# Kernel optimization log

Measured on AMD Instinct MI355X. Metric: run time of the kernel, lower is better.

## Reference

```python
import jax, jax.numpy as jnp
import numpy as np

NDIM = 3        # coordinate dimensionality
KS = 3          # kernel size per dim (odd)
DIL = 0.05      # dilation (spacing between kernel cells)
MAXD = 1.0      # max_distance cap on SDF values
G = 64          # SDF grid resolution per dim
NSDF = 8        # number of SDF grids
OUT = 32        # out_channels
K = KS ** NDIM  # 27 kernel cells
CELL = 0.031    # grid cell size -> grid extent ~2.0


def _kernel_offsets():
    r = (jnp.arange(KS, dtype=jnp.float32) - KS // 2) * DIL
    ox, oy, oz = jnp.meshgrid(r, r, r, indexing='ij')
    return jnp.stack([ox.ravel(), oy.ravel(), oz.ravel()], -1)  # [K,3]


def _rot_inv(q, v):
    # rotate v by the inverse of quaternion q (xyzw layout), broadcasting
    u = -q[..., :3]
    w = q[..., 3:4]
    c = jnp.cross(u, v)
    return v + 2.0 * jnp.cross(u, c + w * v)


def setup_inputs() -> dict:
    key = jax.random.key(0)
    ks = jax.random.split(key, 8)
    B, N, M = 2, 50000, 4
    extent = G * CELL  # ~2.0, local grid extent
    locs = jax.random.uniform(ks[0], (B, N, NDIM), jnp.float32) * extent
    idxs = jax.random.randint(ks[1], (B, M), 0, NSDF).astype(jnp.int32)
    trans = jax.random.uniform(ks[2], (B, M, NDIM), jnp.float32) * 0.2
    quat = jax.random.normal(ks[3], (B, M, 4), jnp.float32)
    quat = quat / jnp.linalg.norm(quat, axis=-1, keepdims=True)
    poses = jnp.concatenate([trans, quat], axis=-1)  # [B,M,7] = trans + quat(xyzw)
    scales = jax.random.uniform(ks[4], (B, M), jnp.float32) + 0.5
    sdf_grid = jax.random.normal(ks[5], (NSDF, G, G, G), jnp.float32) * 0.3 + 0.2
    cell_sizes = jnp.full((NSDF,), CELL, jnp.float32)
    weight = jax.random.normal(ks[6], (OUT, K), jnp.float32) * 0.1
    bias = jax.random.normal(ks[7], (OUT,), jnp.float32) * 0.1
    return dict(locs=locs, idxs=idxs, poses=poses, scales=scales,
                sdf_grid=sdf_grid, cell_sizes=cell_sizes, weight=weight, bias=bias)


def _convsdf(locs, idxs, poses, scales, sdf_grid, cell_sizes, weight, bias):
    offs = _kernel_offsets()                                  # [K,3]
    p = locs[:, :, None, :] + offs[None, None, :, :]          # [B,N,K,3] kernel-cell points
    t = poses[:, :, :NDIM]                                    # [B,M,3]
    q = poses[:, :, NDIM:]                                    # [B,M,4]
    # transform each kernel-cell point into each SDF's local frame
    r = p[:, :, :, None, :] - t[:, None, None, :, :]          # [B,N,K,M,3]
    r = _rot_inv(q[:, None, None, :, :], r)
    sc = scales[:, None, None, :, None]                       # [B,1,1,M,1]
    r = r / sc
    cs = cell_sizes[idxs][:, None, None, :, None]             # [B,1,1,M,1]
    gc = r / cs - 0.5                                         # grid coords (values at cell centers)
    inb = jnp.all((r >= 0.0) & (r <= G * cs), axis=-1)        # [B,N,K,M] inside grid?
    gcc = jnp.clip(gc, 0.0, G - 1.0)
    i0 = jnp.clip(jnp.floor(gcc), 0.0, G - 2.0).astype(jnp.int32)
    fr = gcc - i0.astype(jnp.float32)
    flat = sdf_grid.reshape(-1)
    jb = idxs.astype(jnp.int32)[:, None, None, :]             # [B,1,1,M]
    val = jnp.zeros(inb.shape, jnp.float32)
    # trilinear interpolation: 8 corner gathers
    for dx in (0, 1):
        wx = fr[..., 0] if dx else 1.0 - fr[..., 0]
        for dy in (0, 1):
            wy = fr[..., 1] if dy else 1.0 - fr[..., 1]
            for dz in (0, 1):
                wz = fr[..., 2] if dz else 1.0 - fr[..., 2]
                fi = ((jb * G + i0[..., 0] + dx) * G + i0[..., 1] + dy) * G + i0[..., 2] + dz
                val = val + wx * wy * wz * jnp.take(flat, fi)
    # scaled SDF value; out-of-grid -> max_distance, then min over objects, cap
    val = jnp.where(inb, val * sc[..., 0], MAXD)
    d = jnp.minimum(jnp.min(val, axis=-1), MAXD)              # [B,N,K]
    return jnp.einsum('bnk,ok->bno', d, weight) + bias        # [B,N,OUT]


def reference(locs, idxs, poses, scales, sdf_grid, cell_sizes, weight, bias):
    return _convsdf(locs, idxs, poses, scales, sdf_grid, cell_sizes, weight, bias)
```

## Files before the change

kernel.cpp:

```cpp
#include <hip/hip_runtime.h>
#include <hip/hip_fp16.h>
#include <math.h>

#define KK 27
#define MM 4
#define OUTC 32
#define GG 64
#define GG3 (GG * GG * GG)
#define DILF 0.05f
#define MAXDF 1.0f
#define MU 4e-3f

static __device__ inline bool exact_inb(float lx, float ly, float lz,
                                        float ox, float oy, float oz,
                                        float tx, float ty, float tz,
                                        float qx, float qy, float qz, float qw,
                                        float sc, float gcs) {
#pragma clang fp contract(off)
    float px = lx + ox, py = ly + oy, pz = lz + oz;
    float vx = px - tx, vy = py - ty, vz = pz - tz;
    float ux = -qx, uy = -qy, uz = -qz;
    float cx = uy * vz - uz * vy;
    float cy = uz * vx - ux * vz;
    float cz = ux * vy - uy * vx;
    float twx = cx + qw * vx;
    float twy = cy + qw * vy;
    float twz = cz + qw * vz;
    float rx = vx + 2.0f * (uy * twz - uz * twy);
    float ry = vy + 2.0f * (uz * twx - ux * twz);
    float rz = vz + 2.0f * (ux * twy - uy * twx);
    rx = rx / sc; ry = ry / sc; rz = rz / sc;
    return (rx >= 0.0f) & (rx <= gcs) & (ry >= 0.0f) & (ry <= gcs) &
           (rz >= 0.0f) & (rz <= gcs);
}

__global__ __launch_bounds__(256) void repack_kernel(
    const float* __restrict__ sdf, const int* __restrict__ idxs,
    uint2* __restrict__ quad, int nslots) {
    const int j = blockIdx.y;
    __shared__ int ref;
    if (threadIdx.x == 0) {
        int r = 0;
        for (int s = 0; s < nslots; ++s) r |= (idxs[s] == j) ? 1 : 0;
        ref = r;
    }
    __syncthreads();
    if (!ref) return;

    int i = blockIdx.x * 256 + threadIdx.x;
    int x = i >> 12, y = (i >> 6) & 63, z = i & 63;
    int xp = min(x + 1, 63), zp = min(z + 1, 63);
    const float* g = sdf + (size_t)j * GG3;
    float v000 = g[(x * GG + y) * GG + z];
    float v001 = g[(x * GG + y) * GG + zp];
    float v100 = g[(xp * GG + y) * GG + z];
    float v101 = g[(xp * GG + y) * GG + zp];
    __half2 h0 = __floats2half2_rn(v000, v001);
    __half2 h1 = __floats2half2_rn(v100, v101);
    uint2 o;
    o.x = *(unsigned int*)&h0;
    o.y = *(unsigned int*)&h1;
    quad[(size_t)j * GG3 + i] = o;
}

__global__ __launch_bounds__(256) void convsdf_quad_kernel(
    const float* __restrict__ locs, const int* __restrict__ idxs,
    const float* __restrict__ poses, const float* __restrict__ scales,
    const uint2* __restrict__ quad, const float* __restrict__ cells,
    const float* __restrict__ weight, const float* __restrict__ bias,
    float* __restrict__ out, int N) {
    __shared__ float4 s_ro[MM][KK];
    __shared__ float4 s_off[KK];
    __shared__ float4 s_wT4[KK * OUTC / 4];
    __shared__ float  s_bias[OUTC];
    __shared__ float  s_t[MM][3];
    __shared__ float  s_q[MM][4];
    __shared__ float  s_sc[MM];
    __shared__ float  s_gcs[MM];
    __shared__ float  s_invscs[MM];
    __shared__ int    s_goff[MM];

    const int b = blockIdx.y;
    const int tid = threadIdx.x;

    float* s_wT = (float*)s_wT4;
    for (int i = tid; i < KK * OUTC; i += 256) {
        int k = i >> 5, o = i & 31;
        s_wT[i] = weight[o * KK + k];
    }
    if (tid < OUTC) s_bias[tid] = bias[tid];
    if (tid < KK) {
        int kx = tid / 9, ky = (tid / 3) % 3, kz = tid % 3;
        s_off[tid] = make_float4((float)(kx - 1) * DILF, (float)(ky - 1) * DILF,
                                 (float)(kz - 1) * DILF, 0.0f);
    }
    if (tid >= 128 && tid < 128 + MM) {
        int m = tid - 128;
        const float* pp = poses + (b * MM + m) * 7;
        float sc = scales[b * MM + m];
        int gi = idxs[b * MM + m];
        float cs = cells[gi];
        s_t[m][0] = pp[0]; s_t[m][1] = pp[1]; s_t[m][2] = pp[2];
        s_q[m][0] = pp[3]; s_q[m][1] = pp[4]; s_q[m][2] = pp[5]; s_q[m][3] = pp[6];
        s_sc[m] = sc;
        s_gcs[m] = (float)GG * cs;
        s_invscs[m] = 1.0f / (sc * cs);
        s_goff[m] = gi * GG3;
    }
    __syncthreads();

    if (tid < MM * KK) {
        int m = tid / KK, k = tid - m * KK;
        float4 off = s_off[k];
        float qx = s_q[m][0], qy = s_q[m][1], qz = s_q[m][2], qw = s_q[m][3];
        float ux = -qx, uy = -qy, uz = -qz;
        float vx = off.x, vy = off.y, vz = off.z;
        float cx = uy * vz - uz * vy + qw * vx;
        float cy = uz * vx - ux * vz + qw * vy;
        float cz = ux * vy - uy * vx + qw * vz;
        float rx = vx + 2.0f * (uy * cz - uz * cy);
        float ry = vy + 2.0f * (uz * cx - ux * cz);
        float rz = vz + 2.0f * (ux * cy - uy * cx);
        float f = s_invscs[m];
        s_ro[m][k] = make_float4(rx * f, ry * f, rz * f, 0.0f);
    }
    __syncthreads();

    const int pl = tid >> 2;
    const int m  = tid & 3;
    const int n  = blockIdx.x * 64 + pl;
    if (n >= N) return;

    const float* lp = locs + (size_t)(b * N + n) * 3;
    float lx = lp[0], ly = lp[1], lz = lp[2];

    float tx = s_t[m][0], ty = s_t[m][1], tz = s_t[m][2];
    float qx = s_q[m][0], qy = s_q[m][1], qz = s_q[m][2], qw = s_q[m][3];
    float sc = s_sc[m], gcs = s_gcs[m];
    float bux, buy, buz;
    {
        float vx = lx - tx, vy = ly - ty, vz = lz - tz;
        float ux = -qx, uy = -qy, uz = -qz;
        float cx = uy * vz - uz * vy + qw * vx;
        float cy = uz * vx - ux * vz + qw * vy;
        float cz = ux * vy - uy * vx + qw * vz;
        float rx = vx + 2.0f * (uy * cz - uz * cy);
        float ry = vy + 2.0f * (uz * cx - ux * cz);
        float rz = vz + 2.0f * (ux * cy - uy * cx);
        float f = s_invscs[m];
        bux = rx * f; buy = ry * f; buz = rz * f;
    }
    const uint2* qg = quad + s_goff[m];

    float acc[8];
#pragma unroll
    for (int j = 0; j < 8; ++j) acc[j] = s_bias[m * 8 + j];

#pragma unroll 3
    for (int k = 0; k < KK; ++k) {
        float4 ro = s_ro[m][k];
        float ux = bux + ro.x;
        float uy = buy + ro.y;
        float uz = buz + ro.z;
        float mn = fminf(fminf(ux, uy), uz);
        float mx = fmaxf(fmaxf(ux, uy), uz);
        bool inb = (mn >= 0.0f) & (mx <= 64.0f);
        float a0 = fminf(fminf(fabsf(ux), fabsf(uy)), fabsf(uz));
        float a1 = fminf(fminf(fabsf(ux - 64.0f), fabsf(uy - 64.0f)),
                         fabsf(uz - 64.0f));
        if (fminf(a0, a1) < MU) {
            float4 ofk = s_off[k];
            inb = exact_inb(lx, ly, lz, ofk.x, ofk.y, ofk.z,
                            tx, ty, tz, qx, qy, qz, qw, sc, gcs);
        }
        float v = MAXDF;
        if (inb) {
            float gx = fminf(fmaxf(ux - 0.5f, 0.0f), 63.0f);
            float gy = fminf(fmaxf(uy - 0.5f, 0.0f), 63.0f);
            float gz = fminf(fmaxf(uz - 0.5f, 0.0f), 63.0f);
            int ix = min((int)gx, 62);
            int iy = min((int)gy, 62);
            int iz = min((int)gz, 62);
            float fx = gx - (float)ix;
            float fy = gy - (float)iy;
            float fz = gz - (float)iz;
            int base = (ix * GG + iy) * GG + iz;
            uint2 qa = qg[base];
            uint2 qb = qg[base + GG];
            float2 az  = __half22float2(*(__half2*)&qa.x);
            float2 axz = __half22float2(*(__half2*)&qa.y);
            float2 bz  = __half22float2(*(__half2*)&qb.x);
            float2 bxz = __half22float2(*(__half2*)&qb.y);
            float c00 = az.x  + fz * (az.y  - az.x);
            float c10 = axz.x + fz * (axz.y - axz.x);
            float c01 = bz.x  + fz * (bz.y  - bz.x);
            float c11 = bxz.x + fz * (bxz.y - bxz.x);
            float c0 = c00 + fy * (c01 - c00);
            float c1 = c10 + fy * (c11 - c10);
            v = (c0 + fx * (c1 - c0)) * sc;
        }
        float dk = v;
        dk = fminf(dk, __shfl_xor(dk, 1, 4));
        dk = fminf(dk, __shfl_xor(dk, 2, 4));
        float4 w0 = s_wT4[k * (OUTC / 4) + m * 2 + 0];
        float4 w1 = s_wT4[k * (OUTC / 4) + m * 2 + 1];
        acc[0] += dk * w0.x; acc[1] += dk * w0.y;
        acc[2] += dk * w0.z; acc[3] += dk * w0.w;
        acc[4] += dk * w1.x; acc[5] += dk * w1.y;
        acc[6] += dk * w1.z; acc[7] += dk * w1.w;
    }

    float* op = out + (size_t)(b * N + n) * OUTC + m * 8;
    *(float4*)&op[0] = make_float4(acc[0], acc[1], acc[2], acc[3]);
    *(float4*)&op[4] = make_float4(acc[4], acc[5], acc[6], acc[7]);
}

__global__ __launch_bounds__(256) void convsdf_direct_kernel(
    const float* __restrict__ locs, const int* __restrict__ idxs,
    const float* __restrict__ poses, const float* __restrict__ scales,
    const float* __restrict__ sdf, const float* __restrict__ cells,
    const float* __restrict__ weight, const float* __restrict__ bias,
    float* __restrict__ out, int N) {
    __shared__ float4 s_ro[MM][KK];
    __shared__ float4 s_off[KK];
    __shared__ float4 s_wT4[KK * OUTC / 4];
    __shared__ float  s_bias[OUTC];
    __shared__ float  s_t[MM][3];
    __shared__ float  s_q[MM][4];
    __shared__ float  s_sc[MM];
    __shared__ float  s_gcs[MM];
    __shared__ float  s_invscs[MM];
    __shared__ int    s_goff[MM];

    const int b = blockIdx.y;
    const int tid = threadIdx.x;

    float* s_wT = (float*)s_wT4;
    for (int i = tid; i < KK * OUTC; i += 256) {
        int k = i >> 5, o = i & 31;
        s_wT[i] = weight[o * KK + k];
    }
    if (tid < OUTC) s_bias[tid] = bias[tid];
    if (tid < KK) {
        int kx = tid / 9, ky = (tid / 3) % 3, kz = tid % 3;
        s_off[tid] = make_float4((float)(kx - 1) * DILF, (float)(ky - 1) * DILF,
                                 (float)(kz - 1) * DILF, 0.0f);
    }
    if (tid >= 128 && tid < 128 + MM) {
        int m = tid - 128;
        const float* pp = poses + (b * MM + m) * 7;
        float sc = scales[b * MM + m];
        int gi = idxs[b * MM + m];
        float cs = cells[gi];
        s_t[m][0] = pp[0]; s_t[m][1] = pp[1]; s_t[m][2] = pp[2];
        s_q[m][0] = pp[3]; s_q[m][1] = pp[4]; s_q[m][2] = pp[5]; s_q[m][3] = pp[6];
        s_sc[m] = sc;
        s_gcs[m] = (float)GG * cs;
        s_invscs[m] = 1.0f / (sc * cs);
        s_goff[m] = gi * GG3;
    }
    __syncthreads();

    if (tid < MM * KK) {
        int m = tid / KK, k = tid - m * KK;
        float4 off = s_off[k];
        float qx = s_q[m][0], qy = s_q[m][1], qz = s_q[m][2], qw = s_q[m][3];
        float ux = -qx, uy = -qy, uz = -qz;
        float vx = off.x, vy = off.y, vz = off.z;
        float cx = uy * vz - uz * vy + qw * vx;
        float cy = uz * vx - ux * vz + qw * vy;
        float cz = ux * vy - uy * vx + qw * vz;
        float rx = vx + 2.0f * (uy * cz - uz * cy);
        float ry = vy + 2.0f * (uz * cx - ux * cz);
        float rz = vz + 2.0f * (ux * cy - uy * cx);
        float f = s_invscs[m];
        s_ro[m][k] = make_float4(rx * f, ry * f, rz * f, 0.0f);
    }
    __syncthreads();

    const int pl = tid >> 2;
    const int m  = tid & 3;
    const int n  = blockIdx.x * 64 + pl;
    if (n >= N) return;

    const float* lp = locs + (size_t)(b * N + n) * 3;
    float lx = lp[0], ly = lp[1], lz = lp[2];

    float tx = s_t[m][0], ty = s_t[m][1], tz = s_t[m][2];
    float qx = s_q[m][0], qy = s_q[m][1], qz = s_q[m][2], qw = s_q[m][3];
    float sc = s_sc[m], gcs = s_gcs[m];
    float bux, buy, buz;
    {
        float vx = lx - tx, vy = ly - ty, vz = lz - tz;
        float ux = -qx, uy = -qy, uz = -qz;
        float cx = uy * vz - uz * vy + qw * vx;
        float cy = uz * vx - ux * vz + qw * vy;
        float cz = ux * vy - uy * vx + qw * vz;
        float rx = vx + 2.0f * (uy * cz - uz * cy);
        float ry = vy + 2.0f * (uz * cx - ux * cz);
        float rz = vz + 2.0f * (ux * cy - uy * cx);
        float f = s_invscs[m];
        bux = rx * f; buy = ry * f; buz = rz * f;
    }
    const float* gbase = sdf + s_goff[m];

    float acc[8];
#pragma unroll
    for (int j = 0; j < 8; ++j) acc[j] = s_bias[m * 8 + j];

#pragma unroll 3
    for (int k = 0; k < KK; ++k) {
        float4 ro = s_ro[m][k];
        float ux = bux + ro.x;
        float uy = buy + ro.y;
        float uz = buz + ro.z;
        float mn = fminf(fminf(ux, uy), uz);
        float mx = fmaxf(fmaxf(ux, uy), uz);
        bool inb = (mn >= 0.0f) & (mx <= 64.0f);
        float a0 = fminf(fminf(fabsf(ux), fabsf(uy)), fabsf(uz));
        float a1 = fminf(fminf(fabsf(ux - 64.0f), fabsf(uy - 64.0f)),
                         fabsf(uz - 64.0f));
        if (fminf(a0, a1) < MU) {
            float4 ofk = s_off[k];
            inb = exact_inb(lx, ly, lz, ofk.x, ofk.y, ofk.z,
                            tx, ty, tz, qx, qy, qz, qw, sc, gcs);
        }
        float v = MAXDF;
        if (inb) {
            float gx = fminf(fmaxf(ux - 0.5f, 0.0f), 63.0f);
            float gy = fminf(fmaxf(uy - 0.5f, 0.0f), 63.0f);
            float gz = fminf(fmaxf(uz - 0.5f, 0.0f), 63.0f);
            int ix = min((int)gx, 62);
            int iy = min((int)gy, 62);
            int iz = min((int)gz, 62);
            float fx = gx - (float)ix;
            float fy = gy - (float)iy;
            float fz = gz - (float)iz;
            const float* g = gbase + ((ix * GG + iy) * GG + iz);
            float v000 = g[0], v001 = g[1];
            float v010 = g[GG], v011 = g[GG + 1];
            float v100 = g[GG * GG], v101 = g[GG * GG + 1];
            float v110 = g[GG * GG + GG], v111 = g[GG * GG + GG + 1];
            float c00 = v000 + fz * (v001 - v000);
            float c01 = v010 + fz * (v011 - v010);
            float c10 = v100 + fz * (v101 - v100);
            float c11 = v110 + fz * (v111 - v110);
            float c0 = c00 + fy * (c01 - c00);
            float c1 = c10 + fy * (c11 - c10);
            v = (c0 + fx * (c1 - c0)) * sc;
        }
        float dk = v;
        dk = fminf(dk, __shfl_xor(dk, 1, 4));
        dk = fminf(dk, __shfl_xor(dk, 2, 4));
        float4 w0 = s_wT4[k * (OUTC / 4) + m * 2 + 0];
        float4 w1 = s_wT4[k * (OUTC / 4) + m * 2 + 1];
        acc[0] += dk * w0.x; acc[1] += dk * w0.y;
        acc[2] += dk * w0.z; acc[3] += dk * w0.w;
        acc[4] += dk * w1.x; acc[5] += dk * w1.y;
        acc[6] += dk * w1.z; acc[7] += dk * w1.w;
    }

    float* op = out + (size_t)(b * N + n) * OUTC + m * 8;
    *(float4*)&op[0] = make_float4(acc[0], acc[1], acc[2], acc[3]);
    *(float4*)&op[4] = make_float4(acc[4], acc[5], acc[6], acc[7]);
}

extern "C" void kernel_launch(void* const* d_in, const int* in_sizes, int n_in,
                              void* d_out, int out_size, void* d_ws, size_t ws_size,
                              hipStream_t stream) {
    const float* locs   = (const float*)d_in[0];
    const int*   idxs   = (const int*)d_in[1];
    const float* poses  = (const float*)d_in[2];
    const float* scales = (const float*)d_in[3];
    const float* sdf    = (const float*)d_in[4];
    const float* cells  = (const float*)d_in[5];
    const float* weight = (const float*)d_in[6];
    const float* bias   = (const float*)d_in[7];
    float* out = (float*)d_out;

    int B = in_sizes[1] / MM;
    int N = in_sizes[0] / (3 * B);
    int NSDF = in_sizes[4] / GG3;
    int nslots = in_sizes[1];

    size_t quad_bytes = (size_t)NSDF * GG3 * 8;
    dim3 grid((N + 63) / 64, B);

    if (ws_size >= quad_bytes) {
        uint2* quad = (uint2*)d_ws;
        dim3 gridR(GG3 / 256, NSDF);
        repack_kernel<<<gridR, 256, 0, stream>>>(sdf, idxs, quad, nslots);
        convsdf_quad_kernel<<<grid, 256, 0, stream>>>(locs, idxs, poses, scales,
                                                      quad, cells, weight, bias,
                                                      out, N);
    } else {
        convsdf_direct_kernel<<<grid, 256, 0, stream>>>(locs, idxs, poses,
                                                        scales, sdf, cells,
                                                        weight, bias, out, N);
    }
}
```

Before: 35.26 us.

## Repack SDF into z-pair half2 layout with four 4-byte gathers per sample

The repack now stores only (z, z+1) half2 pairs, one 4-byte word per cell, instead of an 8-byte quad that also held the x+1 neighbours. This halves the repack write traffic and workspace size. In exchange, each interpolation issues four 4-byte gathers instead of two 8-byte ones, so there are more memory instructions per sample. The near-boundary test that decides whether to run the exact in-bounds check is also rewritten to use the min/max already computed, which removes several abs/min operations.

Result: faster. 34.54 us (-2.0%).

```diff
diff --git a/kernel.cpp b/kernel.cpp
--- a/kernel.cpp
+++ b/kernel.cpp
@@ -36,7 +36,7 @@
 
 __global__ __launch_bounds__(256) void repack_kernel(
     const float* __restrict__ sdf, const int* __restrict__ idxs,
-    uint2* __restrict__ quad, int nslots) {
+    unsigned int* __restrict__ zp, int nslots) {
     const int j = blockIdx.y;
     __shared__ int ref;
     if (threadIdx.x == 0) {
@@ -48,25 +48,18 @@
     if (!ref) return;
 
     int i = blockIdx.x * 256 + threadIdx.x;
-    int x = i >> 12, y = (i >> 6) & 63, z = i & 63;
-    int xp = min(x + 1, 63), zp = min(z + 1, 63);
+    int z = i & 63;
     const float* g = sdf + (size_t)j * GG3;
-    float v000 = g[(x * GG + y) * GG + z];
-    float v001 = g[(x * GG + y) * GG + zp];
-    float v100 = g[(xp * GG + y) * GG + z];
-    float v101 = g[(xp * GG + y) * GG + zp];
-    __half2 h0 = __floats2half2_rn(v000, v001);
-    __half2 h1 = __floats2half2_rn(v100, v101);
-    uint2 o;
-    o.x = *(unsigned int*)&h0;
-    o.y = *(unsigned int*)&h1;
-    quad[(size_t)j * GG3 + i] = o;
-}
-
-__global__ __launch_bounds__(256) void convsdf_quad_kernel(
+    float v0 = g[i];
+    float v1 = g[z == 63 ? i : i + 1];
+    __half2 h = __floats2half2_rn(v0, v1);
+    zp[(size_t)j * GG3 + i] = *(unsigned int*)&h;
+}
+
+__global__ __launch_bounds__(256) void convsdf_zp_kernel(
     const float* __restrict__ locs, const int* __restrict__ idxs,
     const float* __restrict__ poses, const float* __restrict__ scales,
-    const uint2* __restrict__ quad, const float* __restrict__ cells,
+    const unsigned int* __restrict__ zp, const float* __restrict__ cells,
     const float* __restrict__ weight, const float* __restrict__ bias,
     float* __restrict__ out, int N) {
     __shared__ float4 s_ro[MM][KK];
@@ -150,7 +143,7 @@
         float f = s_invscs[m];
         bux = rx * f; buy = ry * f; buz = rz * f;
     }
-    const uint2* qg = quad + s_goff[m];
+    const unsigned int* zg = zp + s_goff[m];
 
     float acc[8];
 #pragma unroll
@@ -165,10 +158,8 @@
         float mn = fminf(fminf(ux, uy), uz);
         float mx = fmaxf(fmaxf(ux, uy), uz);
         bool inb = (mn >= 0.0f) & (mx <= 64.0f);
-        float a0 = fminf(fminf(fabsf(ux), fabsf(uy)), fabsf(uz));
-        float a1 = fminf(fminf(fabsf(ux - 64.0f), fabsf(uy - 64.0f)),
-                         fabsf(uz - 64.0f));
-        if (fminf(a0, a1) < MU) {
+        if ((mn > -MU) & (mx < 64.0f + MU) &
+            ((mn < MU) | (mx > 64.0f - MU))) {
             float4 ofk = s_off[k];
             inb = exact_inb(lx, ly, lz, ofk.x, ofk.y, ofk.z,
                             tx, ty, tz, qx, qy, qz, qw, sc, gcs);
@@ -185,16 +176,18 @@
             float fy = gy - (float)iy;
             float fz = gz - (float)iz;
             int base = (ix * GG + iy) * GG + iz;
-            uint2 qa = qg[base];
-            uint2 qb = qg[base + GG];
-            float2 az  = __half22float2(*(__half2*)&qa.x);
-            float2 axz = __half22float2(*(__half2*)&qa.y);
-            float2 bz  = __half22float2(*(__half2*)&qb.x);
-            float2 bxz = __half22float2(*(__half2*)&qb.y);
-            float c00 = az.x  + fz * (az.y  - az.x);
-            float c10 = axz.x + fz * (axz.y - axz.x);
-            float c01 = bz.x  + fz * (bz.y  - bz.x);
-            float c11 = bxz.x + fz * (bxz.y - bxz.x);
+            unsigned int r00 = zg[base];
+            unsigned int r01 = zg[base + GG];
+            unsigned int r10 = zg[base + GG * GG];
+            unsigned int r11 = zg[base + GG * GG + GG];
+            float2 p00 = __half22float2(*(__half2*)&r00);
+            float2 p01 = __half22float2(*(__half2*)&r01);
+            float2 p10 = __half22float2(*(__half2*)&r10);
+            float2 p11 = __half22float2(*(__half2*)&r11);
+            float c00 = p00.x + fz * (p00.y - p00.x);
+            float c01 = p01.x + fz * (p01.y - p01.x);
+            float c10 = p10.x + fz * (p10.y - p10.x);
+            float c11 = p11.x + fz * (p11.y - p11.x);
             float c0 = c00 + fy * (c01 - c00);
             float c1 = c10 + fy * (c11 - c10);
             v = (c0 + fx * (c1 - c0)) * sc;
@@ -317,10 +310,8 @@
         float mn = fminf(fminf(ux, uy), uz);
         float mx = fmaxf(fmaxf(ux, uy), uz);
         bool inb = (mn >= 0.0f) & (mx <= 64.0f);
-        float a0 = fminf(fminf(fabsf(ux), fabsf(uy)), fabsf(uz));
-        float a1 = fminf(fminf(fabsf(ux - 64.0f), fabsf(uy - 64.0f)),
-                         fabsf(uz - 64.0f));
-        if (fminf(a0, a1) < MU) {
+        if ((mn > -MU) & (mx < 64.0f + MU) &
+            ((mn < MU) | (mx > 64.0f - MU))) {
             float4 ofk = s_off[k];
             inb = exact_inb(lx, ly, lz, ofk.x, ofk.y, ofk.z,
                             tx, ty, tz, qx, qy, qz, qw, sc, gcs);
@@ -383,16 +374,16 @@
     int NSDF = in_sizes[4] / GG3;
     int nslots = in_sizes[1];
 
-    size_t quad_bytes = (size_t)NSDF * GG3 * 8;
+    size_t zp_bytes = (size_t)NSDF * GG3 * 4;
     dim3 grid((N + 63) / 64, B);
 
-    if (ws_size >= quad_bytes) {
-        uint2* quad = (uint2*)d_ws;
+    if (ws_size >= zp_bytes) {
+        unsigned int* zpg = (unsigned int*)d_ws;
         dim3 gridR(GG3 / 256, NSDF);
-        repack_kernel<<<gridR, 256, 0, stream>>>(sdf, idxs, quad, nslots);
-        convsdf_quad_kernel<<<grid, 256, 0, stream>>>(locs, idxs, poses, scales,
-                                                      quad, cells, weight, bias,
-                                                      out, N);
+        repack_kernel<<<gridR, 256, 0, stream>>>(sdf, idxs, zpg, nslots);
+        convsdf_zp_kernel<<<grid, 256, 0, stream>>>(locs, idxs, poses, scales,
+                                                    zpg, cells, weight, bias,
+                                                    out, N);
     } else {
         convsdf_direct_kernel<<<grid, 256, 0, stream>>>(locs, idxs, poses,
                                                         scales, sdf, cells,
```
